# Performance work log

Measured on AMD Instinct MI355X. Metric: run time of the kernel, lower is better.

Reference implementation:

```python
import jax, jax.numpy as jnp
import numpy as np
import math

EMBED_DIM = 1024
BATCH = 4
SEQ = 2048


def setup_inputs() -> dict:
    key = jax.random.key(0)
    ks = jax.random.split(key, 7)
    d = EMBED_DIM
    s = 1.0 / math.sqrt(d)
    x = jax.random.normal(ks[0], (BATCH, SEQ, d), dtype=jnp.float32)
    Wq = jax.random.normal(ks[1], (d, d), dtype=jnp.float32) * s
    Wk = jax.random.normal(ks[2], (d, d), dtype=jnp.float32) * s
    Wv = jax.random.normal(ks[3], (d, d), dtype=jnp.float32) * s
    bq = jax.random.normal(ks[4], (d,), dtype=jnp.float32) * 0.01
    bk = jax.random.normal(ks[5], (d,), dtype=jnp.float32) * 0.01
    bv = jax.random.normal(ks[6], (d,), dtype=jnp.float32) * 0.01
    return {"x": x, "Wq": Wq, "bq": bq, "Wk": Wk, "bk": bk, "Wv": Wv, "bv": bv}


def reference(x, Wq, bq, Wk, bk, Wv, bv):
    # q/k/v: [B, S, D] linear projections (weights stored as [in, out])
    q = jnp.einsum('bsd,de->bse', x, Wq) + bq
    k = jnp.einsum('bsd,de->bse', x, Wk) + bk
    v = jnp.einsum('bsd,de->bse', x, Wv) + bv
    scale = jnp.sqrt(jnp.asarray(x.shape[-1], dtype=x.dtype))
    # full O(S^2) score matrix, as in the original (non-fused) attention
    attn_scores = jnp.einsum('bqd,bkd->bqk', q, k) / scale
    attn_probs = jax.nn.softmax(attn_scores, axis=-1)
    # lxa.strassen(attn_probs, v) is a (Strassen) matmul: same math as matmul
    return jnp.einsum('bqk,bkd->bqd', attn_probs, v)
```

## Files before the change

kernel.cpp:

```cpp
#include <hip/hip_runtime.h>
#include <stdint.h>

#define SEQ 2048
#define DIM 1024
#define NB 4
#define MTOT (NB*SEQ)
#define QKVN (3*DIM)

typedef __attribute__((ext_vector_type(8))) short short8;
typedef __attribute__((ext_vector_type(4))) float f32x4;

__device__ __forceinline__ unsigned short f2b(float f) {
    union { float f; unsigned int u; } v; v.f = f;
    return (unsigned short)((v.u + 0x7FFFu + ((v.u >> 16) & 1u)) >> 16);
}

__device__ __forceinline__ void gload_lds16(const unsigned short* g, unsigned short* l) {
    __builtin_amdgcn_global_load_lds(
        (const __attribute__((address_space(1))) void*)g,
        (__attribute__((address_space(3))) void*)l, 16, 0, 0);
}

__device__ __forceinline__ short8 ds128(unsigned addr) {
    short8 r;
    asm volatile("ds_read_b128 %0, %1" : "=v"(r) : "v"(addr));
    return r;
}

#define FENCE_BARRIER do { asm volatile("" ::: "memory"); \
    __builtin_amdgcn_s_barrier(); asm volatile("" ::: "memory"); } while (0)

__device__ __forceinline__ int xcd_swz(int bid, int nwg) {
    if (nwg & 7) return bid;
    return (bid & 7) * (nwg >> 3) + (bid >> 3);
}


__global__ __launch_bounds__(256)
void cast_kernel(const float* __restrict__ in, unsigned short* __restrict__ out, int nchunk) {
    int i = blockIdx.x * 256 + threadIdx.x;
    if (i >= nchunk) return;
    float4 a = ((const float4*)in)[i*2];
    float4 b = ((const float4*)in)[i*2+1];
    union { unsigned short u[8]; uint4 v; } r;
    r.u[0]=f2b(a.x); r.u[1]=f2b(a.y); r.u[2]=f2b(a.z); r.u[3]=f2b(a.w);
    r.u[4]=f2b(b.x); r.u[5]=f2b(b.y); r.u[6]=f2b(b.z); r.u[7]=f2b(b.w);
    ((uint4*)out)[i] = r.v;
}

__global__ __launch_bounds__(256)
void transpose_cast_f32(const float* __restrict__ in, unsigned short* __restrict__ out, int R, int C) {
    __shared__ unsigned short tile[64][66];
    int tpc = C >> 6;
    int tr = (blockIdx.x / tpc) << 6;
    int tc = (blockIdx.x % tpc) << 6;
    int t = threadIdx.x;
    #pragma unroll
    for (int i = 0; i < 16; i++) {
        int idx = t + i*256;
        int r = idx >> 6, c = idx & 63;
        tile[r][c] = f2b(in[(size_t)(tr + r)*C + tc + c]);
    }
    __syncthreads();
    #pragma unroll
    for (int i = 0; i < 16; i++) {
        int idx = t + i*256;
        int r = idx >> 6, c = idx & 63;
        out[(size_t)(tc + r)*R + tr + c] = tile[c][r];
    }
}

__global__ __launch_bounds__(256)
void transpose_b16(const unsigned short* __restrict__ in0, size_t sIn, int ldin,
                   unsigned short* __restrict__ out0, size_t sOut, int ldout, int tpc) {
    const unsigned short* in = in0 + sIn * blockIdx.y;
    unsigned short* out = out0 + sOut * blockIdx.y;
    __shared__ unsigned short tile[64][66];
    int tr = ((int)blockIdx.x / tpc) << 6;
    int tc = ((int)blockIdx.x % tpc) << 6;
    int t = threadIdx.x;
    #pragma unroll
    for (int i = 0; i < 16; i++) {
        int idx = t + i*256;
        int r = idx >> 6, c = idx & 63;
        tile[r][c] = in[(size_t)(tr + r)*ldin + tc + c];
    }
    __syncthreads();
    #pragma unroll
    for (int i = 0; i < 16; i++) {
        int idx = t + i*256;
        int r = idx >> 6, c = idx & 63;
        out[(size_t)(tc + r)*ldout + tr + c] = tile[c][r];
    }
}

__global__ __launch_bounds__(256)
void bias_concat(const float* __restrict__ bq, const float* __restrict__ bk,
                 const float* __restrict__ bv, float* __restrict__ o) {
    int i = blockIdx.x*256 + threadIdx.x;
    float v = (i < DIM) ? bq[i] : ((i < 2*DIM) ? bk[i-DIM] : bv[i-2*DIM]);
    o[i] = v;
}


__device__ __forceinline__ void stage1(const unsigned short* __restrict__ Xb, int ldx,
                                       unsigned short* dstBase, int h, int k0,
                                       int tid, int wid) {
    int srow = tid >> 3;
    int scol = ((tid & 7) ^ (srow & 7)) << 3;
    const unsigned short* g = Xb + (size_t)(h*128 + srow)*ldx + k0 + scol;
    unsigned short* d = dstBase + h*8192 + wid*512;
    gload_lds16(g, d);
    gload_lds16(g + (size_t)64*ldx, d + 4096);
}

#define RD_A(BUF) do { _Pragma("unroll") for (int mf = 0; mf < 4; ++mf) { \
    fa[mf][0] = ds128(As0 + (BUF)*16384u + aRow + mf*2048u + c0); \
    fa[mf][1] = ds128(As0 + (BUF)*16384u + aRow + mf*2048u + c1); } } while (0)

#define RD_B(BUF, QN) do { _Pragma("unroll") for (int nf = 0; nf < 2; ++nf) { \
    fb[nf][0] = ds128(Bs0 + (BUF)*32768u + (QN)*16384u + bRow + nf*2048u + c0); \
    fb[nf][1] = ds128(Bs0 + (BUF)*32768u + (QN)*16384u + bRow + nf*2048u + c1); } } while (0)

#define MMA_PH(QN) do { \
    asm volatile("s_waitcnt lgkmcnt(0)" ::: "memory"); \
    __builtin_amdgcn_sched_barrier(0); \
    __builtin_amdgcn_s_setprio(1); \
    _Pragma("unroll") for (int mf = 0; mf < 4; ++mf) \
      _Pragma("unroll") for (int nf = 0; nf < 2; ++nf) \
        _Pragma("unroll") for (int ks = 0; ks < 2; ++ks) \
          acc[QN][mf][nf] = __builtin_amdgcn_mfma_f32_16x16x32_bf16( \
              fa[mf][ks], fb[nf][ks], acc[QN][mf][nf], 0, 0, 0); \
    __builtin_amdgcn_s_setprio(0); \
} while (0)

template<int MODE>
__global__ __launch_bounds__(512, 2)
void gemm4p(const unsigned short* __restrict__ A, int lda, size_t sA,
            const unsigned short* __restrict__ Bt, int ldb, size_t sB,
            const float* __restrict__ bias,
            void* __restrict__ Cout, int ldc, size_t sC,
            int N, int K)
{
    __shared__ __align__(16) unsigned short As[2][8192];
    __shared__ __align__(16) unsigned short Bs[2][16384];
    int nbn = N >> 8;
    int bid = xcd_swz((int)blockIdx.x, (int)gridDim.x);
    int bm = bid / nbn, bn = bid % nbn;
    int bz = blockIdx.y;
    int tid = threadIdx.x;
    int lane = tid & 63;
    int wid  = tid >> 6;
    int wm = (wid >> 2) & 1;
    int wn = wid & 3;
    int rlo = lane & 15;
    int shi = lane >> 4;

    unsigned As0 = (unsigned)(uintptr_t)&As[0][0];
    unsigned Bs0 = (unsigned)(uintptr_t)&Bs[0][0];
    unsigned c0 = (unsigned)(((shi     ^ rlo) & 7) * 16);
    unsigned c1 = (unsigned)((((4+shi) ^ rlo) & 7) * 16);
    unsigned aRow = (unsigned)((wm*64 + rlo) * 128);
    unsigned bRow = (unsigned)((wn*32 + rlo) * 128);

    f32x4 acc[2][4][2];
    #pragma unroll
    for (int a = 0; a < 2; a++)
        #pragma unroll
        for (int b = 0; b < 4; b++)
            #pragma unroll
            for (int c = 0; c < 2; c++)
                acc[a][b][c] = (f32x4){0.f,0.f,0.f,0.f};

    const unsigned short* Ab = A + sA*bz + (size_t)(bm*128)*lda;
    const unsigned short* Bb = Bt + sB*bz + (size_t)(bn*256)*ldb;

    stage1(Ab, lda, &As[0][0], 0, 0,  tid, wid);
    stage1(Bb, ldb, &Bs[0][0], 0, 0,  tid, wid);
    stage1(Bb, ldb, &Bs[0][0], 1, 0,  tid, wid);
    stage1(Ab, lda, &As[1][0], 0, 64, tid, wid);
    stage1(Bb, ldb, &Bs[1][0], 0, 64, tid, wid);
    __builtin_amdgcn_sched_barrier(0);
    asm volatile("s_waitcnt vmcnt(4)" ::: "memory");
    FENCE_BARRIER;

    short8 fa[4][2], fb[2][2];
    int nt = K >> 6;
    int nit = nt >> 1;

    for (int it = 0; it < nit; ++it) {
        int kO  = (2*it + 1) << 6;
        int kE2 = (2*it + 2 < nt) ? (2*it + 2) << 6 : 0;
        int kO2 = (2*it + 3 < nt) ? (2*it + 3) << 6 : 0;

        RD_A(0); RD_B(0, 0);
        stage1(Bb, ldb, &Bs[1][0], 1, kO, tid, wid);
        asm volatile("s_waitcnt lgkmcnt(8)" ::: "memory");
        FENCE_BARRIER; MMA_PH(0); FENCE_BARRIER;
        RD_B(0, 1);
        stage1(Ab, lda, &As[0][0], 0, kE2, tid, wid);
        stage1(Bb, ldb, &Bs[0][0], 0, kE2, tid, wid);
        __builtin_amdgcn_sched_barrier(0);
        asm volatile("s_waitcnt vmcnt(4)" ::: "memory");
        FENCE_BARRIER; MMA_PH(1); FENCE_BARRIER;
        RD_A(1); RD_B(1, 0);
        stage1(Bb, ldb, &Bs[0][0], 1, kE2, tid, wid);
        asm volatile("s_waitcnt lgkmcnt(8)" ::: "memory");
        FENCE_BARRIER; MMA_PH(0); FENCE_BARRIER;
        RD_B(1, 1);
        stage1(Ab, lda, &As[1][0], 0, kO2, tid, wid);
        stage1(Bb, ldb, &Bs[1][0], 0, kO2, tid, wid);
        __builtin_amdgcn_sched_barrier(0);
        asm volatile("s_waitcnt vmcnt(4)" ::: "memory");
        FENCE_BARRIER; MMA_PH(1); FENCE_BARRIER;
    }

    asm volatile("s_waitcnt vmcnt(0)" ::: "memory");

    int r0 = shi << 2;
    unsigned short* Cu = (unsigned short*)Cout + sC*bz;
    float* Cf = (float*)Cout + sC*bz;
    #pragma unroll
    for (int qn = 0; qn < 2; ++qn)
        #pragma unroll
        for (int mf = 0; mf < 4; ++mf)
            #pragma unroll
            for (int nf = 0; nf < 2; ++nf) {
                int col = bn*256 + qn*128 + wn*32 + nf*16 + rlo;
                float badd = (MODE == 0) ? bias[col] : 0.f;
                #pragma unroll
                for (int r = 0; r < 4; ++r) {
                    int row = bm*128 + wm*64 + mf*16 + r0 + r;
                    float v = acc[qn][mf][nf][r];
                    if (MODE == 0) Cu[(size_t)row*ldc + col] = f2b(v + badd);
                    else           Cf[(size_t)row*ldc + col] = v;
                }
            }
}

__global__ __launch_bounds__(256)
void softmax_kernel(float* __restrict__ S, float scl) {
    int row = blockIdx.x;
    float* srow = S + (size_t)row * SEQ;
    int t = threadIdx.x;
    float4 v0 = ((const float4*)srow)[t*2];
    float4 v1 = ((const float4*)srow)[t*2+1];
    float x[8] = {v0.x*scl,v0.y*scl,v0.z*scl,v0.w*scl,v1.x*scl,v1.y*scl,v1.z*scl,v1.w*scl};
    float m = fmaxf(fmaxf(fmaxf(x[0],x[1]),fmaxf(x[2],x[3])),
                    fmaxf(fmaxf(x[4],x[5]),fmaxf(x[6],x[7])));
    #pragma unroll
    for (int off = 32; off; off >>= 1) m = fmaxf(m, __shfl_xor(m, off));
    __shared__ float redm[4], reds[4];
    int w = t >> 6;
    if ((t & 63) == 0) redm[w] = m;
    __syncthreads();
    m = fmaxf(fmaxf(redm[0], redm[1]), fmaxf(redm[2], redm[3]));
    float e[8]; float s = 0.f;
    #pragma unroll
    for (int i = 0; i < 8; i++) { e[i] = __expf(x[i] - m); s += e[i]; }
    #pragma unroll
    for (int off = 32; off; off >>= 1) s += __shfl_xor(s, off);
    if ((t & 63) == 0) reds[w] = s;
    __syncthreads();
    float inv = 1.0f / (reds[0]+reds[1]+reds[2]+reds[3]);
    union { unsigned short u[8]; uint4 v; } r;
    #pragma unroll
    for (int i = 0; i < 8; i++) r.u[i] = f2b(e[i] * inv);
    ((uint4*)srow)[t] = r.v;
}

extern "C" void kernel_launch(void* const* d_in, const int* in_sizes, int n_in,
                              void* d_out, int out_size, void* d_ws, size_t ws_size,
                              hipStream_t stream)
{
    (void)in_sizes; (void)n_in; (void)out_size;
    const float* x  = (const float*)d_in[0];
    const float* Wq = (const float*)d_in[1];
    const float* bq = (const float*)d_in[2];
    const float* Wk = (const float*)d_in[3];
    const float* bk = (const float*)d_in[4];
    const float* Wv = (const float*)d_in[5];
    const float* bv = (const float*)d_in[6];
    float* out = (float*)d_out;

    unsigned short* qkv = (unsigned short*)d_ws;
    unsigned short* vt  = qkv + (size_t)MTOT*QKVN;
    float* biasc = (float*)(vt + (size_t)NB*DIM*SEQ);
    char* ovl = (char*)biasc + 65536;
    unsigned short* xb    = (unsigned short*)ovl;
    unsigned short* wqkvt = xb + (size_t)MTOT*DIM;
    float* scores = (float*)ovl;

    size_t base = (size_t)MTOT*QKVN*2 + (size_t)NB*DIM*SEQ*2 + 65536;
    int bpp = 1;
    if (base + 4*(size_t)SEQ*SEQ*4 <= ws_size) bpp = 4;
    else if (base + 2*(size_t)SEQ*SEQ*4 <= ws_size) bpp = 2;

    cast_kernel<<<MTOT*DIM/8/256, 256, 0, stream>>>(x, xb, MTOT*DIM/8);
    transpose_cast_f32<<<256, 256, 0, stream>>>(Wq, wqkvt,             DIM, DIM);
    transpose_cast_f32<<<256, 256, 0, stream>>>(Wk, wqkvt + DIM*DIM,   DIM, DIM);
    transpose_cast_f32<<<256, 256, 0, stream>>>(Wv, wqkvt + 2*DIM*DIM, DIM, DIM);
    bias_concat<<<QKVN/256, 256, 0, stream>>>(bq, bk, bv, biasc);

    gemm4p<0><<<dim3((MTOT/128)*(QKVN/256)), 512, 0, stream>>>(
        xb, DIM, 0, wqkvt, DIM, 0, biasc, qkv, QKVN, 0, QKVN, DIM);

    transpose_b16<<<dim3((SEQ/64)*(DIM/64), NB), 256, 0, stream>>>(
        qkv + 2*DIM, (size_t)SEQ*QKVN, QKVN, vt, (size_t)DIM*SEQ, SEQ, DIM/64);

    const float scl = 1.0f / 32.0f;
    for (int p = 0; p < NB; p += bpp) {
        const unsigned short* qp = qkv + (size_t)p*SEQ*QKVN;
        gemm4p<1><<<dim3((SEQ/128)*(SEQ/256), bpp), 512, 0, stream>>>(
            qp,       QKVN, (size_t)SEQ*QKVN,
            qp + DIM, QKVN, (size_t)SEQ*QKVN,
            nullptr, scores, SEQ, (size_t)SEQ*SEQ, SEQ, DIM);
        softmax_kernel<<<bpp*SEQ, 256, 0, stream>>>(scores, scl);
        gemm4p<1><<<dim3((SEQ/128)*(DIM/256), bpp), 512, 0, stream>>>(
            (const unsigned short*)scores, 2*SEQ, (size_t)SEQ*2*SEQ,
            vt + (size_t)p*DIM*SEQ,        SEQ,   (size_t)DIM*SEQ,
            nullptr, out + (size_t)p*SEQ*DIM, DIM, (size_t)SEQ*DIM, DIM, SEQ);
    }
}
```

Measured before the change: 189.4 us.

## Triple-buffer GEMM LDS pipeline and merge weight transpose-cast launches

Replaces the double-buffered two-phase GEMM main loop with a three-stage LDS ring, prefetching two k-tiles ahead and issuing all MMAs for a k-step after a single barrier. This aims to hide global-to-LDS latency better and cut barrier count per k-step. It raises LDS use to about 144 KB per block and keeps more B fragments live in registers. The three weight transpose-cast launches are also folded into one grid launch to trim launch overhead.

```diff
diff --git a/kernel.cpp b/kernel.cpp
--- a/kernel.cpp
+++ b/kernel.cpp
@@ -49,24 +49,27 @@
 }
 
 __global__ __launch_bounds__(256)
-void transpose_cast_f32(const float* __restrict__ in, unsigned short* __restrict__ out, int R, int C) {
+void transpose_cast3(const float* __restrict__ w0, const float* __restrict__ w1,
+                     const float* __restrict__ w2, unsigned short* __restrict__ out) {
+    const float* in = (blockIdx.y == 0) ? w0 : (blockIdx.y == 1) ? w1 : w2;
+    unsigned short* o = out + (size_t)blockIdx.y * DIM * DIM;
     __shared__ unsigned short tile[64][66];
-    int tpc = C >> 6;
-    int tr = (blockIdx.x / tpc) << 6;
-    int tc = (blockIdx.x % tpc) << 6;
+    int tpc = DIM >> 6;
+    int tr = ((int)blockIdx.x / tpc) << 6;
+    int tc = ((int)blockIdx.x % tpc) << 6;
     int t = threadIdx.x;
     #pragma unroll
     for (int i = 0; i < 16; i++) {
         int idx = t + i*256;
         int r = idx >> 6, c = idx & 63;
-        tile[r][c] = f2b(in[(size_t)(tr + r)*C + tc + c]);
+        tile[r][c] = f2b(in[(size_t)(tr + r)*DIM + tc + c]);
     }
     __syncthreads();
     #pragma unroll
     for (int i = 0; i < 16; i++) {
         int idx = t + i*256;
         int r = idx >> 6, c = idx & 63;
-        out[(size_t)(tc + r)*R + tr + c] = tile[c][r];
+        o[(size_t)(tc + r)*DIM + tr + c] = tile[c][r];
     }
 }
 
@@ -114,36 +117,24 @@
     gload_lds16(g + (size_t)64*ldx, d + 4096);
 }
 
-#define RD_A(BUF) do { _Pragma("unroll") for (int mf = 0; mf < 4; ++mf) { \
-    fa[mf][0] = ds128(As0 + (BUF)*16384u + aRow + mf*2048u + c0); \
-    fa[mf][1] = ds128(As0 + (BUF)*16384u + aRow + mf*2048u + c1); } } while (0)
-
-#define RD_B(BUF, QN) do { _Pragma("unroll") for (int nf = 0; nf < 2; ++nf) { \
-    fb[nf][0] = ds128(Bs0 + (BUF)*32768u + (QN)*16384u + bRow + nf*2048u + c0); \
-    fb[nf][1] = ds128(Bs0 + (BUF)*32768u + (QN)*16384u + bRow + nf*2048u + c1); } } while (0)
-
-#define MMA_PH(QN) do { \
-    asm volatile("s_waitcnt lgkmcnt(0)" ::: "memory"); \
-    __builtin_amdgcn_sched_barrier(0); \
-    __builtin_amdgcn_s_setprio(1); \
-    _Pragma("unroll") for (int mf = 0; mf < 4; ++mf) \
-      _Pragma("unroll") for (int nf = 0; nf < 2; ++nf) \
-        _Pragma("unroll") for (int ks = 0; ks < 2; ++ks) \
-          acc[QN][mf][nf] = __builtin_amdgcn_mfma_f32_16x16x32_bf16( \
-              fa[mf][ks], fb[nf][ks], acc[QN][mf][nf], 0, 0, 0); \
-    __builtin_amdgcn_s_setprio(0); \
-} while (0)
+#define RD_A(BUFB) do { _Pragma("unroll") for (int mf = 0; mf < 4; ++mf) { \
+    fa[mf][0] = ds128(As0 + (BUFB) + aRow + mf*2048u + c0); \
+    fa[mf][1] = ds128(As0 + (BUFB) + aRow + mf*2048u + c1); } } while (0)
+
+#define RD_B(DST, BUFB, QN) do { _Pragma("unroll") for (int nf = 0; nf < 2; ++nf) { \
+    DST[nf][0] = ds128(Bs0 + (BUFB) + (QN)*16384u + bRow + nf*2048u + c0); \
+    DST[nf][1] = ds128(Bs0 + (BUFB) + (QN)*16384u + bRow + nf*2048u + c1); } } while (0)
 
 template<int MODE>
 __global__ __launch_bounds__(512, 2)
-void gemm4p(const unsigned short* __restrict__ A, int lda, size_t sA,
+void gemm3b(const unsigned short* __restrict__ A, int lda, size_t sA,
             const unsigned short* __restrict__ Bt, int ldb, size_t sB,
             const float* __restrict__ bias,
             void* __restrict__ Cout, int ldc, size_t sC,
             int N, int K)
 {
-    __shared__ __align__(16) unsigned short As[2][8192];
-    __shared__ __align__(16) unsigned short Bs[2][16384];
+    __shared__ __align__(16) unsigned short As[3][8192];
+    __shared__ __align__(16) unsigned short Bs[3][16384];
     int nbn = N >> 8;
     int bid = xcd_swz((int)blockIdx.x, (int)gridDim.x);
     int bm = bid / nbn, bn = bid % nbn;
@@ -180,39 +171,53 @@
     stage1(Bb, ldb, &Bs[0][0], 1, 0,  tid, wid);
     stage1(Ab, lda, &As[1][0], 0, 64, tid, wid);
     stage1(Bb, ldb, &Bs[1][0], 0, 64, tid, wid);
+    stage1(Bb, ldb, &Bs[1][0], 1, 64, tid, wid);
     __builtin_amdgcn_sched_barrier(0);
-    asm volatile("s_waitcnt vmcnt(4)" ::: "memory");
+    asm volatile("s_waitcnt vmcnt(6)" ::: "memory");
     FENCE_BARRIER;
 
-    short8 fa[4][2], fb[2][2];
+    short8 fa[4][2], fb0[2][2], fb1[2][2];
     int nt = K >> 6;
-    int nit = nt >> 1;
-
-    for (int it = 0; it < nit; ++it) {
-        int kO  = (2*it + 1) << 6;
-        int kE2 = (2*it + 2 < nt) ? (2*it + 2) << 6 : 0;
-        int kO2 = (2*it + 3 < nt) ? (2*it + 3) << 6 : 0;
-
-        RD_A(0); RD_B(0, 0);
-        stage1(Bb, ldb, &Bs[1][0], 1, kO, tid, wid);
+    int cur = 0, n1 = 1, n2 = 2;
+
+    for (int p = 0; p < nt; ++p) {
+        int kN = (p + 2 < nt) ? (p + 2) << 6 : 0;
+        unsigned curA = (unsigned)cur * 16384u;
+        unsigned curB = (unsigned)cur * 32768u;
+
+        RD_A(curA);
+        RD_B(fb0, curB, 0);
+        RD_B(fb1, curB, 1);
+        stage1(Ab, lda, &As[n2][0], 0, kN, tid, wid);
+        stage1(Bb, ldb, &Bs[n2][0], 0, kN, tid, wid);
+        stage1(Bb, ldb, &Bs[n2][0], 1, kN, tid, wid);
         asm volatile("s_waitcnt lgkmcnt(8)" ::: "memory");
-        FENCE_BARRIER; MMA_PH(0); FENCE_BARRIER;
-        RD_B(0, 1);
-        stage1(Ab, lda, &As[0][0], 0, kE2, tid, wid);
-        stage1(Bb, ldb, &Bs[0][0], 0, kE2, tid, wid);
         __builtin_amdgcn_sched_barrier(0);
-        asm volatile("s_waitcnt vmcnt(4)" ::: "memory");
-        FENCE_BARRIER; MMA_PH(1); FENCE_BARRIER;
-        RD_A(1); RD_B(1, 0);
-        stage1(Bb, ldb, &Bs[0][0], 1, kE2, tid, wid);
-        asm volatile("s_waitcnt lgkmcnt(8)" ::: "memory");
-        FENCE_BARRIER; MMA_PH(0); FENCE_BARRIER;
-        RD_B(1, 1);
-        stage1(Ab, lda, &As[1][0], 0, kO2, tid, wid);
-        stage1(Bb, ldb, &Bs[1][0], 0, kO2, tid, wid);
+        asm volatile("s_waitcnt vmcnt(6)" ::: "memory");
+        FENCE_BARRIER;
+        asm volatile("s_waitcnt lgkmcnt(0)" ::: "memory");
         __builtin_amdgcn_sched_barrier(0);
-        asm volatile("s_waitcnt vmcnt(4)" ::: "memory");
-        FENCE_BARRIER; MMA_PH(1); FENCE_BARRIER;
+        __builtin_amdgcn_s_setprio(1);
+        #pragma unroll
+        for (int mf = 0; mf < 4; ++mf)
+            #pragma unroll
+            for (int nf = 0; nf < 2; ++nf)
+                #pragma unroll
+                for (int ks = 0; ks < 2; ++ks)
+                    acc[0][mf][nf] = __builtin_amdgcn_mfma_f32_16x16x32_bf16(
+                        fa[mf][ks], fb0[nf][ks], acc[0][mf][nf], 0, 0, 0);
+        #pragma unroll
+        for (int mf = 0; mf < 4; ++mf)
+            #pragma unroll
+            for (int nf = 0; nf < 2; ++nf)
+                #pragma unroll
+                for (int ks = 0; ks < 2; ++ks)
+                    acc[1][mf][nf] = __builtin_amdgcn_mfma_f32_16x16x32_bf16(
+                        fa[mf][ks], fb1[nf][ks], acc[1][mf][nf], 0, 0, 0);
+        __builtin_amdgcn_s_setprio(0);
+        FENCE_BARRIER;
+
+        int t = cur; cur = n1; n1 = n2; n2 = t;
     }
 
     asm volatile("s_waitcnt vmcnt(0)" ::: "memory");
@@ -297,12 +302,10 @@
     else if (base + 2*(size_t)SEQ*SEQ*4 <= ws_size) bpp = 2;
 
     cast_kernel<<<MTOT*DIM/8/256, 256, 0, stream>>>(x, xb, MTOT*DIM/8);
-    transpose_cast_f32<<<256, 256, 0, stream>>>(Wq, wqkvt,             DIM, DIM);
-    transpose_cast_f32<<<256, 256, 0, stream>>>(Wk, wqkvt + DIM*DIM,   DIM, DIM);
-    transpose_cast_f32<<<256, 256, 0, stream>>>(Wv, wqkvt + 2*DIM*DIM, DIM, DIM);
+    transpose_cast3<<<dim3(256, 3), 256, 0, stream>>>(Wq, Wk, Wv, wqkvt);
     bias_concat<<<QKVN/256, 256, 0, stream>>>(bq, bk, bv, biasc);
 
-    gemm4p<0><<<dim3((MTOT/128)*(QKVN/256)), 512, 0, stream>>>(
+    gemm3b<0><<<dim3((MTOT/128)*(QKVN/256)), 512, 0, stream>>>(
         xb, DIM, 0, wqkvt, DIM, 0, biasc, qkv, QKVN, 0, QKVN, DIM);
 
     transpose_b16<<<dim3((SEQ/64)*(DIM/64), NB), 256, 0, stream>>>(
@@ -311,12 +314,12 @@
     const float scl = 1.0f / 32.0f;
     for (int p = 0; p < NB; p += bpp) {
         const unsigned short* qp = qkv + (size_t)p*SEQ*QKVN;
-        gemm4p<1><<<dim3((SEQ/128)*(SEQ/256), bpp), 512, 0, stream>>>(
+        gemm3b<1><<<dim3((SEQ/128)*(SEQ/256), bpp), 512, 0, stream>>>(
             qp,       QKVN, (size_t)SEQ*QKVN,
             qp + DIM, QKVN, (size_t)SEQ*QKVN,
             nullptr, scores, SEQ, (size_t)SEQ*SEQ, SEQ, DIM);
         softmax_kernel<<<bpp*SEQ, 256, 0, stream>>>(scores, scl);
-        gemm4p<1><<<dim3((SEQ/128)*(DIM/256), bpp), 512, 0, stream>>>(
+        gemm3b<1><<<dim3((SEQ/128)*(DIM/256), bpp), 512, 0, stream>>>(
             (const unsigned short*)scores, 2*SEQ, (size_t)SEQ*2*SEQ,
             vt + (size_t)p*DIM*SEQ,        SEQ,   (size_t)DIM*SEQ,
             nullptr, out + (size_t)p*SEQ*DIM, DIM, (size_t)SEQ*DIM, DIM, SEQ);
```

Measured after the change: 193.8 us. 2.3% more time.
